# Performance work log

Measured on AMD Instinct MI355X. Metric: run time of the kernel, lower is better.

The kernel has to match this reference:

```python
import jax, jax.numpy as jnp
import numpy as np

N_ATOMS = 512
BATCH = 32


def _get_segments(n):
    # shifted pairs (k, k+1), all combinations of 2 rows, drop pairs where end1 == start2
    pairs = np.stack([np.arange(n - 1), np.arange(1, n)], axis=1)  # (n-1, 2)
    i, j = np.triu_indices(n - 1, k=1)
    seg = np.concatenate([pairs[i], pairs[j]], axis=1)  # (M, 4)
    seg = seg[seg[:, 1] != seg[:, 2]]
    return seg.astype(np.int32)  # (129795, 4) for n=512


def setup_inputs() -> dict:
    key = jax.random.key(0)
    x = jax.random.normal(key, (BATCH, N_ATOMS, 3), dtype=jnp.float32) * 5.0
    segments = jnp.asarray(_get_segments(N_ATOMS))
    return {"x": x, "segments": segments}


def _nnorm(v):
    return v / jnp.linalg.norm(v, axis=-1, keepdims=True)


def reference(x, segments):
    n = N_ATOMS
    x = x.reshape(-1, n, 3)
    B = x.shape[0]
    smat = x[:, segments]                       # (B, S, 4, 3) gather
    S = smat.shape[1]
    # displacements between the two segment endpoints pairs: d_{ab} = p_{2+b} - p_a
    disp = _nnorm((-smat[:, :, :2, None, :] + smat[:, :, None, 2:, :]).reshape(B, S, 4, 3))
    crosses = _nnorm(jnp.cross(disp[:, :, [0, 1, 3, 2]], disp[:, :, [1, 3, 2, 0]]))
    omega = jnp.arcsin(
        jnp.clip(jnp.sum(crosses * crosses[:, :, [1, 2, 3, 0]], axis=-1), -1.0, 1.0)
    ).sum(axis=2)                               # (B, S)
    signs = jnp.sign(
        jnp.sum(
            jnp.cross(_nnorm(smat[:, :, 3] - smat[:, :, 2]), _nnorm(smat[:, :, 1] - smat[:, :, 0]))
            * disp[:, :, 0],
            axis=-1,
        )
    )
    wr = (omega * signs) / (2.0 * jnp.pi)       # (B, S)
    # scatter into adjacency matrix (sequential sets: second overrides first, like torch)
    adj = jnp.zeros((B, n, n), dtype=x.dtype)
    adj = adj.at[:, segments[:, 0], segments[:, 2]].set(wr)
    adj = adj.at[:, segments[:, 1], segments[:, 3]].set(wr)
    return adj + jnp.swapaxes(adj, 1, 2)
```

## Files before the change

### kernel.cpp

```cpp
#include <hip/hip_runtime.h>
#include <math.h>

#define N 512
#define TILE 32
#define INV2PI 0.15915494309189535f

__device__ __forceinline__ float2 pset(float a, float b) { return make_float2(a, b); }
__device__ __forceinline__ float2 psplat(float a) { return make_float2(a, a); }
__device__ __forceinline__ float2 p_sub(float2 a, float2 b) { return make_float2(a.x - b.x, a.y - b.y); }
__device__ __forceinline__ float2 p_mul(float2 a, float2 b) { return make_float2(a.x * b.x, a.y * b.y); }
__device__ __forceinline__ float2 p_fma(float2 a, float2 b, float2 c) {
    return make_float2(fmaf(a.x, b.x, c.x), fmaf(a.y, b.y, c.y));
}
__device__ __forceinline__ float2 p_fmsub(float2 a, float2 b, float2 c, float2 d) {
    return make_float2(fmaf(a.x, b.x, -(c.x * d.x)), fmaf(a.y, b.y, -(c.y * d.y)));
}
__device__ __forceinline__ float2 p_rsq(float2 a) {
    return make_float2(__builtin_amdgcn_rsqf(a.x), __builtin_amdgcn_rsqf(a.y));
}

struct F3P { float2 x, y, z; };

__device__ __forceinline__ F3P pp_sub(F3P a, F3P b) {
    return {p_sub(a.x, b.x), p_sub(a.y, b.y), p_sub(a.z, b.z)};
}
__device__ __forceinline__ F3P pp_cross(F3P a, F3P b) {
    F3P c;
    c.x = p_fmsub(a.y, b.z, a.z, b.y);
    c.y = p_fmsub(a.z, b.x, a.x, b.z);
    c.z = p_fmsub(a.x, b.y, a.y, b.x);
    return c;
}
__device__ __forceinline__ float2 pp_dot(F3P a, F3P b) {
    return p_fma(a.x, b.x, p_fma(a.y, b.y, p_mul(a.z, b.z)));
}

__device__ __forceinline__ float2 p_asin_clamped(float2 t) {
    float2 ax = make_float2(fminf(fabsf(t.x), 1.f), fminf(fabsf(t.y), 1.f));
    float2 p = p_fma(ax, psplat(-0.0187293f), psplat(0.0742610f));
    p = p_fma(ax, p, psplat(-0.2121144f));
    p = p_fma(ax, p, psplat(1.5707288f));
    float sx = __builtin_amdgcn_sqrtf(1.0f - ax.x);
    float sy = __builtin_amdgcn_sqrtf(1.0f - ax.y);
    float rx = fmaf(-sx, p.x, 1.5707963267948966f);
    float ry = fmaf(-sy, p.y, 1.5707963267948966f);
    return make_float2(copysignf(rx, t.x), copysignf(ry, t.y));
}

__device__ __forceinline__ float2 wr_core2(F3P p0, F3P p1, F3P p2, F3P p3) {
    F3P d0 = pp_sub(p2, p0), d1 = pp_sub(p3, p0), d2 = pp_sub(p2, p1), d3 = pp_sub(p3, p1);

    F3P c0 = pp_cross(d0, d1);
    F3P c1 = pp_cross(d1, d3);
    F3P c2 = pp_cross(d3, d2);
    F3P c3 = pp_cross(d2, d0);

    float2 q0 = pp_dot(c0, c0);
    float2 q1 = pp_dot(c1, c1);
    float2 q2 = pp_dot(c2, c2);
    float2 q3 = pp_dot(c3, c3);

    float2 t01 = p_mul(pp_dot(c0, c1), p_rsq(p_mul(q0, q1)));
    float2 t12 = p_mul(pp_dot(c1, c2), p_rsq(p_mul(q1, q2)));
    float2 t23 = p_mul(pp_dot(c2, c3), p_rsq(p_mul(q2, q3)));
    float2 t30 = p_mul(pp_dot(c3, c0), p_rsq(p_mul(q3, q0)));

    float2 a01 = p_asin_clamped(t01), a12 = p_asin_clamped(t12);
    float2 a23 = p_asin_clamped(t23), a30 = p_asin_clamped(t30);
    float2 omega = make_float2(a01.x + a12.x + a23.x + a30.x,
                               a01.y + a12.y + a23.y + a30.y);

    float2 svn = pp_dot(d1, c3);
    float ox = __int_as_float(__float_as_int(omega.x) ^
                              (__float_as_int(svn.x) & 0x80000000));
    float oy = __int_as_float(__float_as_int(omega.y) ^
                              (__float_as_int(svn.y) & 0x80000000));
    return make_float2(ox * -INV2PI, oy * -INV2PI);
}

__device__ __forceinline__ F3P pack_pt(const float4* __restrict__ xs4, int i0, int i1) {
    float4 a = xs4[i0];
    float4 b = xs4[i1];
    F3P r;
    r.x = pset(a.x, b.x);
    r.y = pset(a.y, b.y);
    r.z = pset(a.z, b.z);
    return r;
}

__device__ __forceinline__ F3P splat_pt(const float4* __restrict__ xs4, int i) {
    float4 a = xs4[i];
    F3P r;
    r.x = psplat(a.x);
    r.y = psplat(a.y);
    r.z = psplat(a.z);
    return r;
}

__device__ __forceinline__ void elem_idx(int gi, int gj, int& a, int& b, bool& valid) {
    const int lo = min(gi, gj), hi = max(gi, gj);
    const bool z = (lo == 0);
    a = z ? 0 : (lo - 1);
    b = z ? min(hi, 510) : (hi - 1);
    valid = z ? ((hi >= 2) && (hi <= 510)) : (hi >= lo + 2);
}

__global__ __launch_bounds__(256) void writhe_tile(const float* __restrict__ x,
                                                   float* __restrict__ out) {
    __shared__ __align__(16) float4 xs4[N];
    __shared__ float ts[TILE][TILE + 1];

    const int batch = blockIdx.y;

    {
        const float4* src = (const float4*)(x + (size_t)batch * (N * 3));
        float* xsf = (float*)xs4;
        for (int i = threadIdx.x; i < (N * 3) / 4; i += blockDim.x) {
            float4 g = src[i];
            const int base = 4 * i;
            float vv[4] = {g.x, g.y, g.z, g.w};
#pragma unroll
            for (int j = 0; j < 4; ++j) {
                const int e = base + j;
                xsf[(e / 3) * 4 + (e % 3)] = vv[j];
            }
        }
    }

    int p = blockIdx.x;
    int ti = 0;
    while (p >= (N / TILE) - ti) { p -= (N / TILE) - ti; ++ti; }
    const int tj = ti + p;
    const bool diag = (ti == tj);

    __syncthreads();

    float* ob = out + (size_t)batch * (N * N);

    if (ti >= 1 && !diag) {
        const int c = threadIdx.x & 15;
        const int r = threadIdx.x >> 4;
        const int gj0 = tj * TILE + c;
        const int gj1 = gj0 + 16;

        const F3P P2 = pack_pt(xs4, gj0 - 1, gj1 - 1);
        const F3P P3 = pack_pt(xs4, gj0, gj1);

#pragma unroll
        for (int k = 0; k < 2; ++k) {
            const int rr = r + 16 * k;
            const int gi = ti * TILE + rr;
            const F3P P0 = splat_pt(xs4, gi - 1);
            const F3P P1 = splat_pt(xs4, gi);
            float2 wr = wr_core2(P0, P1, P2, P3);
            const float vx = (gj0 >= gi + 2) ? wr.x : 0.f;
            const float vy = wr.y;
            ob[(size_t)gi * N + gj0] = vx;
            ob[(size_t)gi * N + gj1] = vy;
            ts[rr][c] = vx;
            ts[rr][c + 16] = vy;
        }

        __syncthreads();
#pragma unroll
        for (int k = 0; k < 4; ++k) {
            const int r2 = (threadIdx.x >> 5) + 8 * k;
            const int c2 = threadIdx.x & 31;
            ob[(size_t)(tj * TILE + r2) * N + (ti * TILE + c2)] = ts[c2][r2];
        }
    } else {
        const int c = threadIdx.x & 31;
        const int r0 = threadIdx.x >> 5;
        const int gj = tj * TILE + c;

#pragma unroll
        for (int k = 0; k < 2; ++k) {
            const int rA = r0 + 8 * k;
            const int rB = rA + 16;
            const int giA = ti * TILE + rA;
            const int giB = ti * TILE + rB;

            int aA, bA, aB, bB;
            bool vA, vB;
            elem_idx(giA, gj, aA, bA, vA);
            elem_idx(giB, gj, aB, bB, vB);

            F3P P0 = pack_pt(xs4, aA, aB);
            F3P P1 = pack_pt(xs4, aA + 1, aB + 1);
            F3P P2 = pack_pt(xs4, bA, bB);
            F3P P3 = pack_pt(xs4, bA + 1, bB + 1);

            float2 wr = wr_core2(P0, P1, P2, P3);
            const float vxA = vA ? wr.x : 0.f;
            const float vxB = vB ? wr.y : 0.f;

            ob[(size_t)giA * N + gj] = vxA;
            ob[(size_t)giB * N + gj] = vxB;
            if (!diag) {
                ts[rA][c] = vxA;
                ts[rB][c] = vxB;
            }
        }

        if (!diag) {
            __syncthreads();
#pragma unroll
            for (int k = 0; k < 4; ++k) {
                const int r2 = r0 + 8 * k;
                ob[(size_t)(tj * TILE + r2) * N + (ti * TILE + c)] = ts[c][r2];
            }
        }
    }
}

extern "C" void kernel_launch(void* const* d_in, const int* in_sizes, int n_in,
                              void* d_out, int out_size, void* d_ws, size_t ws_size,
                              hipStream_t stream) {
    const float* x = (const float*)d_in[0];
    float* out = (float*)d_out;
    const int B = in_sizes[0] / (N * 3);

    const int ntiles = N / TILE;
    const int npairs = ntiles * (ntiles + 1) / 2;

    dim3 block(256);
    dim3 grid(npairs, B);
    writhe_tile<<<grid, block, 0, stream>>>(x, out);
}
```

Measured before the change: 79.72 us.

## Simplify writhe cross products and vectorize tile stores with float2/float4

Rewrites the four face-normal cross products using bilinearity: computes d0×v, d0×u and u×v once and derives the remaining two normals by subtraction, with the sign taken from (u×v)·d0. This trims ALU work per pair. The off-diagonal tile path now gives each thread two adjacent columns, so it writes float2 stores directly and float4 stores for the transposed half, reading from a padded shared-memory tile with stride 34. The changes target instruction count and global store transactions, at the risk of small numerical differences from the reassociated cross products.

```diff
diff --git a/kernel.cpp b/kernel.cpp
--- a/kernel.cpp
+++ b/kernel.cpp
@@ -3,6 +3,7 @@
 
 #define N 512
 #define TILE 32
+#define TSTRIDE 34
 #define INV2PI 0.15915494309189535f
 
 __device__ __forceinline__ float2 pset(float a, float b) { return make_float2(a, b); }
@@ -48,12 +49,17 @@
 }
 
 __device__ __forceinline__ float2 wr_core2(F3P p0, F3P p1, F3P p2, F3P p3) {
-    F3P d0 = pp_sub(p2, p0), d1 = pp_sub(p3, p0), d2 = pp_sub(p2, p1), d3 = pp_sub(p3, p1);
-
-    F3P c0 = pp_cross(d0, d1);
-    F3P c1 = pp_cross(d1, d3);
-    F3P c2 = pp_cross(d3, d2);
-    F3P c3 = pp_cross(d2, d0);
+    F3P u = pp_sub(p1, p0);
+    F3P v = pp_sub(p3, p2);
+    F3P d0 = pp_sub(p2, p0);
+
+    F3P c0 = pp_cross(d0, v);
+    F3P c3 = pp_cross(d0, u);
+    F3P w  = pp_cross(u, v);
+    F3P c1 = {p_sub(w.x, c3.x), p_sub(w.y, c3.y), p_sub(w.z, c3.z)};
+    F3P c2 = {p_sub(w.x, c0.x), p_sub(w.y, c0.y), p_sub(w.z, c0.z)};
+
+    float2 svn = pp_dot(w, d0);
 
     float2 q0 = pp_dot(c0, c0);
     float2 q1 = pp_dot(c1, c1);
@@ -70,7 +76,6 @@
     float2 omega = make_float2(a01.x + a12.x + a23.x + a30.x,
                                a01.y + a12.y + a23.y + a30.y);
 
-    float2 svn = pp_dot(d1, c3);
     float ox = __int_as_float(__float_as_int(omega.x) ^
                               (__float_as_int(svn.x) & 0x80000000));
     float oy = __int_as_float(__float_as_int(omega.y) ^
@@ -78,16 +83,16 @@
     return make_float2(ox * -INV2PI, oy * -INV2PI);
 }
 
-__device__ __forceinline__ F3P pack_pt(const float4* __restrict__ xs4, int i0, int i1) {
-    float4 a = xs4[i0];
-    float4 b = xs4[i1];
+__device__ __forceinline__ F3P pack_pt4(float4 a, float4 b) {
     F3P r;
     r.x = pset(a.x, b.x);
     r.y = pset(a.y, b.y);
     r.z = pset(a.z, b.z);
     return r;
 }
-
+__device__ __forceinline__ F3P pack_pt(const float4* __restrict__ xs4, int i0, int i1) {
+    return pack_pt4(xs4[i0], xs4[i1]);
+}
 __device__ __forceinline__ F3P splat_pt(const float4* __restrict__ xs4, int i) {
     float4 a = xs4[i];
     F3P r;
@@ -108,7 +113,7 @@
 __global__ __launch_bounds__(256) void writhe_tile(const float* __restrict__ x,
                                                    float* __restrict__ out) {
     __shared__ __align__(16) float4 xs4[N];
-    __shared__ float ts[TILE][TILE + 1];
+    __shared__ __align__(16) float tsf[TILE * TSTRIDE];
 
     const int batch = blockIdx.y;
 
@@ -138,13 +143,15 @@
     float* ob = out + (size_t)batch * (N * N);
 
     if (ti >= 1 && !diag) {
-        const int c = threadIdx.x & 15;
+        const int cp = threadIdx.x & 15;
         const int r = threadIdx.x >> 4;
-        const int gj0 = tj * TILE + c;
-        const int gj1 = gj0 + 16;
-
-        const F3P P2 = pack_pt(xs4, gj0 - 1, gj1 - 1);
-        const F3P P3 = pack_pt(xs4, gj0, gj1);
+        const int gj0 = tj * TILE + 2 * cp;
+
+        const float4 qa = xs4[gj0 - 1];
+        const float4 qb = xs4[gj0];
+        const float4 qc = xs4[gj0 + 1];
+        const F3P P2 = pack_pt4(qa, qb);
+        const F3P P3 = pack_pt4(qb, qc);
 
 #pragma unroll
         for (int k = 0; k < 2; ++k) {
@@ -154,19 +161,22 @@
             const F3P P1 = splat_pt(xs4, gi);
             float2 wr = wr_core2(P0, P1, P2, P3);
             const float vx = (gj0 >= gi + 2) ? wr.x : 0.f;
-            const float vy = wr.y;
-            ob[(size_t)gi * N + gj0] = vx;
-            ob[(size_t)gi * N + gj1] = vy;
-            ts[rr][c] = vx;
-            ts[rr][c + 16] = vy;
+            const float vy = (gj0 + 1 >= gi + 2) ? wr.y : 0.f;
+            const float2 vv = make_float2(vx, vy);
+            *(float2*)(ob + (size_t)gi * N + gj0) = vv;
+            *(float2*)(tsf + rr * TSTRIDE + 2 * cp) = vv;
         }
 
         __syncthreads();
-#pragma unroll
-        for (int k = 0; k < 4; ++k) {
-            const int r2 = (threadIdx.x >> 5) + 8 * k;
-            const int c2 = threadIdx.x & 31;
-            ob[(size_t)(tj * TILE + r2) * N + (ti * TILE + c2)] = ts[c2][r2];
+        {
+            const int r2 = threadIdx.x & 31;
+            const int g = threadIdx.x >> 5;
+            float4 o;
+            o.x = tsf[(4 * g + 0) * TSTRIDE + r2];
+            o.y = tsf[(4 * g + 1) * TSTRIDE + r2];
+            o.z = tsf[(4 * g + 2) * TSTRIDE + r2];
+            o.w = tsf[(4 * g + 3) * TSTRIDE + r2];
+            *(float4*)(ob + (size_t)(tj * TILE + r2) * N + ti * TILE + 4 * g) = o;
         }
     } else {
         const int c = threadIdx.x & 31;
@@ -197,8 +207,8 @@
             ob[(size_t)giA * N + gj] = vxA;
             ob[(size_t)giB * N + gj] = vxB;
             if (!diag) {
-                ts[rA][c] = vxA;
-                ts[rB][c] = vxB;
+                tsf[rA * TSTRIDE + c] = vxA;
+                tsf[rB * TSTRIDE + c] = vxB;
             }
         }
 
@@ -207,7 +217,7 @@
 #pragma unroll
             for (int k = 0; k < 4; ++k) {
                 const int r2 = r0 + 8 * k;
-                ob[(size_t)(tj * TILE + r2) * N + (ti * TILE + c)] = ts[c][r2];
+                ob[(size_t)(tj * TILE + r2) * N + (ti * TILE + c)] = tsf[c * TSTRIDE + r2];
             }
         }
     }
```

Measured after the change: 79.10 us. Within noise of the previous version (-0.8%).
